# Kernel tuning notes

Hardware: AMD Instinct MI355X
Metric: run time of the kernel (lower is better)

## Reference

```python
import jax, jax.numpy as jnp
import numpy as np

B, T = 64, 256
IN, HID, OUT = 512, 1024, 256
NUM_DOMAINS = 20

def setup_inputs() -> dict:
    key = jax.random.key(0)
    k1, k2, k3, k4 = jax.random.split(key, 4)
    x = jax.random.normal(k1, (B, T, IN), dtype=jnp.float32)
    hetero_info = jax.random.randint(k2, (B, 2), 0, NUM_DOMAINS, dtype=jnp.int64)
    # embedding tables init N(0, 0.02) as in the torch module
    fc1_table = 0.02 * jax.random.normal(k3, (NUM_DOMAINS, IN * HID + HID), dtype=jnp.float32)
    fc2_table = 0.02 * jax.random.normal(k4, (NUM_DOMAINS, HID * OUT + OUT), dtype=jnp.float32)
    return {"x": x, "hetero_info": hetero_info, "fc1_table": fc1_table, "fc2_table": fc2_table}

def reference(x, hetero_info, fc1_table, fc2_table):
    domain_id = hetero_info[:, 0].astype(jnp.int32)
    Bn = domain_id.shape[0]
    fc1_param = fc1_table[domain_id]                     # (B, IN*HID + HID)
    w1 = fc1_param[:, : IN * HID].reshape(Bn, IN, HID)   # (B, IN, HID)
    b1 = fc1_param[:, IN * HID:].reshape(Bn, 1, HID)
    fc2_param = fc2_table[domain_id]                     # (B, HID*OUT + OUT)
    w2 = fc2_param[:, : HID * OUT].reshape(Bn, HID, OUT) # (B, HID, OUT)
    b2 = fc2_param[:, HID * OUT:].reshape(Bn, 1, OUT)
    h = jnp.einsum('bti,bih->bth', x, w1) + b1
    h = jax.nn.gelu(h, approximate=False)  # torch nn.GELU default = exact erf
    out = jnp.einsum('bth,bho->bto', h, w2) + b2
    return out
```

## Files before the change

### kernel.cpp

```cpp
#include <hip/hip_runtime.h>
#include <math.h>

#define B_  64
#define T_  256
#define IN_ 512
#define HID_ 1024
#define OUT_ 256
#define NDOM 20

typedef __bf16 bf16_t;
typedef __bf16 bf16x8 __attribute__((ext_vector_type(8)));
typedef float  f32x4  __attribute__((ext_vector_type(4)));

__device__ __forceinline__ unsigned f2bf_bits(float f) {
    unsigned u = __builtin_bit_cast(unsigned, f);
    return (u + 0x7FFFu + ((u >> 16) & 1u)) >> 16;
}
__device__ __forceinline__ unsigned pack_bf16x2(float x, float y) {
    return f2bf_bits(x) | (f2bf_bits(y) << 16);
}

__device__ __forceinline__ void gl_lds16(const void* g, void* l) {
    __builtin_amdgcn_global_load_lds(
        (const __attribute__((address_space(1))) unsigned*)g,
        (__attribute__((address_space(3))) unsigned*)l,
        16, 0, 0);
}

template<int K, int N>
__global__ __launch_bounds__(256) void cvt_transpose(
    const float* __restrict__ table, bf16_t* __restrict__ Wt, float* __restrict__ BiasOut)
{
    const int d  = blockIdx.z;
    const float* W = table + (size_t)d * ((size_t)K * N + N);
    const int n0 = blockIdx.x * 64;
    const int k0 = blockIdx.y * 64;
    const int tid = threadIdx.x;

    __shared__ float t[64][65];

    #pragma unroll
    for (int r = 0; r < 4; ++r) {
        const int kl = (tid >> 4) + r * 16;
        const int nl = (tid & 15) * 4;
        float4 v = *(const float4*)(W + (size_t)(k0 + kl) * N + n0 + nl);
        t[kl][nl + 0] = v.x; t[kl][nl + 1] = v.y;
        t[kl][nl + 2] = v.z; t[kl][nl + 3] = v.w;
    }
    __syncthreads();

    bf16_t* Wtd = Wt + (size_t)d * K * N;
    #pragma unroll
    for (int r = 0; r < 4; ++r) {
        const int nl = (tid >> 4) + r * 16;
        const int k4 = (tid & 15) * 4;
        uint2 p;
        p.x = pack_bf16x2(t[k4 + 0][nl], t[k4 + 1][nl]);
        p.y = pack_bf16x2(t[k4 + 2][nl], t[k4 + 3][nl]);
        *(uint2*)(Wtd + (size_t)(n0 + nl) * K + k0 + k4) = p;
    }

    if (blockIdx.y == 0 && tid < 64)
        BiasOut[(size_t)d * N + n0 + tid] = W[(size_t)K * N + n0 + tid];
}

__global__ __launch_bounds__(256) void fc1_gemm(
    const float*  __restrict__ X,
    const bf16_t* __restrict__ W1t,
    const float*  __restrict__ Bias,
    const int*    __restrict__ hetero,
    bf16_t*       __restrict__ H)
{
    const int id   = blockIdx.x;
    const int g    = id & 127;
    const int nidx = id >> 7;
    const int b    = g >> 1;
    const int m0   = (g & 1) * 128;
    const int n0   = nidx * 128;
    const int d    = hetero[2 * b];
    const bf16_t* W    = W1t + (size_t)d * HID_ * IN_;
    const float*  bias = Bias + (size_t)d * HID_;

    __shared__ __attribute__((aligned(16))) float  LdsA[128 * 32];
    __shared__ __attribute__((aligned(16))) bf16_t LdsB[128 * 32];

    const int tid  = threadIdx.x;
    const int wave = tid >> 6;
    const int lane = tid & 63;
    const int l16  = lane & 15;
    const int quad = lane >> 4;
    const int wm   = (wave >> 1) * 64;
    const int wn   = (wave & 1) * 64;

    f32x4 acc[4][4] = {};

    for (int kk = 0; kk < IN_; kk += 32) {
        #pragma unroll
        for (int cc = 0; cc < 4; ++cc) {
            const int r0  = wave * 32 + cc * 8;
            const int row = r0 + (lane >> 3);
            const int cs  = (lane & 7) ^ (row & 7);
            gl_lds16(X + ((size_t)(b * 256 + m0 + row) * IN_ + kk + cs * 4),
                     &LdsA[r0 * 32]);
        }
        #pragma unroll
        for (int cc = 0; cc < 2; ++cc) {
            const int r0  = wave * 32 + cc * 16;
            const int row = r0 + (lane >> 2);
            const int cs  = (lane & 3) ^ ((row >> 1) & 3);
            gl_lds16(W + (size_t)(n0 + row) * IN_ + kk + cs * 8,
                     &LdsB[r0 * 32]);
        }
        __syncthreads();

        bf16x8 af[4], bfg[4];
        #pragma unroll
        for (int i = 0; i < 4; ++i) {
            const int r  = wm + i * 16 + l16;
            const int c0 = (quad * 2)     ^ (r & 7);
            const int c1 = (quad * 2 + 1) ^ (r & 7);
            float4 f0 = *(const float4*)&LdsA[r * 32 + c0 * 4];
            float4 f1 = *(const float4*)&LdsA[r * 32 + c1 * 4];
            union { bf16x8 v; unsigned u[4]; } a;
            a.u[0] = pack_bf16x2(f0.x, f0.y);
            a.u[1] = pack_bf16x2(f0.z, f0.w);
            a.u[2] = pack_bf16x2(f1.x, f1.y);
            a.u[3] = pack_bf16x2(f1.z, f1.w);
            af[i] = a.v;
        }
        #pragma unroll
        for (int j = 0; j < 4; ++j) {
            const int r  = wn + j * 16 + l16;
            const int cB = quad ^ ((r >> 1) & 3);
            bfg[j] = *(const bf16x8*)&LdsB[r * 32 + cB * 8];
        }
        #pragma unroll
        for (int i = 0; i < 4; ++i)
            #pragma unroll
            for (int j = 0; j < 4; ++j)
                acc[i][j] = __builtin_amdgcn_mfma_f32_16x16x32_bf16(af[i], bfg[j], acc[i][j], 0, 0, 0);
        __syncthreads();
    }

    #pragma unroll
    for (int j = 0; j < 4; ++j) {
        const int n = n0 + wn + j * 16 + l16;
        const float bia = bias[n];
        #pragma unroll
        for (int i = 0; i < 4; ++i) {
            const int mbase = m0 + wm + i * 16 + quad * 4;
            #pragma unroll
            for (int r = 0; r < 4; ++r) {
                float vv = acc[i][j][r] + bia;
                vv = 0.5f * vv * (1.0f + erff(vv * 0.70710678f));
                H[((size_t)b * 256 + mbase + r) * HID_ + n] = (bf16_t)vv;
            }
        }
    }
}

__global__ __launch_bounds__(256) void fc2_gemm(
    const bf16_t* __restrict__ H,
    const bf16_t* __restrict__ W2t,
    const float*  __restrict__ Bias,
    const int*    __restrict__ hetero,
    float*        __restrict__ Out)
{
    const int id   = blockIdx.x;
    const int g    = id & 255;
    const int nidx = id >> 8;
    const int b    = g >> 2;
    const int m0   = (g & 3) * 64;
    const int n0   = nidx * 64;
    const int d    = hetero[2 * b];
    const bf16_t* W    = W2t + (size_t)d * OUT_ * HID_;
    const float*  bias = Bias + (size_t)d * OUT_;

    __shared__ __attribute__((aligned(16))) bf16_t LdsA[64 * 64];
    __shared__ __attribute__((aligned(16))) bf16_t LdsB[64 * 64];

    const int tid  = threadIdx.x;
    const int wave = tid >> 6;
    const int lane = tid & 63;
    const int l16  = lane & 15;
    const int quad = lane >> 4;
    const int wm   = (wave >> 1) * 32;
    const int wn   = (wave & 1) * 32;

    f32x4 acc[2][2] = {};

    for (int kk = 0; kk < HID_; kk += 64) {
        #pragma unroll
        for (int cc = 0; cc < 2; ++cc) {
            const int r0  = wave * 16 + cc * 8;
            const int row = r0 + (lane >> 3);
            const int cs  = (lane & 7) ^ (row & 7);
            gl_lds16(H + (size_t)(b * 256 + m0 + row) * HID_ + kk + cs * 8,
                     &LdsA[r0 * 64]);
        }
        #pragma unroll
        for (int cc = 0; cc < 2; ++cc) {
            const int r0  = wave * 16 + cc * 8;
            const int row = r0 + (lane >> 3);
            const int cs  = (lane & 7) ^ (row & 7);
            gl_lds16(W + (size_t)(n0 + row) * HID_ + kk + cs * 8,
                     &LdsB[r0 * 64]);
        }
        __syncthreads();

        #pragma unroll
        for (int h = 0; h < 2; ++h) {
            bf16x8 af[2], bfg[2];
            #pragma unroll
            for (int i = 0; i < 2; ++i) {
                const int r = wm + i * 16 + l16;
                const int c = (h * 4 + quad) ^ (r & 7);
                af[i] = *(const bf16x8*)&LdsA[r * 64 + c * 8];
            }
            #pragma unroll
            for (int j = 0; j < 2; ++j) {
                const int r = wn + j * 16 + l16;
                const int c = (h * 4 + quad) ^ (r & 7);
                bfg[j] = *(const bf16x8*)&LdsB[r * 64 + c * 8];
            }
            #pragma unroll
            for (int i = 0; i < 2; ++i)
                #pragma unroll
                for (int j = 0; j < 2; ++j)
                    acc[i][j] = __builtin_amdgcn_mfma_f32_16x16x32_bf16(af[i], bfg[j], acc[i][j], 0, 0, 0);
        }
        __syncthreads();
    }

    #pragma unroll
    for (int j = 0; j < 2; ++j) {
        const int n = n0 + wn + j * 16 + l16;
        const float bia = bias[n];
        #pragma unroll
        for (int i = 0; i < 2; ++i) {
            const int mbase = m0 + wm + i * 16 + quad * 4;
            #pragma unroll
            for (int r = 0; r < 4; ++r) {
                Out[((size_t)b * 256 + mbase + r) * OUT_ + n] = acc[i][j][r] + bia;
            }
        }
    }
}

extern "C" void kernel_launch(void* const* d_in, const int* in_sizes, int n_in,
                              void* d_out, int out_size, void* d_ws, size_t ws_size,
                              hipStream_t stream) {
    const float* x         = (const float*)d_in[0];
    const int*   hetero    = (const int*)d_in[1];
    const float* fc1_table = (const float*)d_in[2];
    const float* fc2_table = (const float*)d_in[3];
    float*       out       = (float*)d_out;

    char* ws = (char*)d_ws;
    bf16_t* W1t = (bf16_t*)(ws);
    bf16_t* W2t = (bf16_t*)(ws + 20971520);
    float*  b1  = (float*)(ws + 31457280);
    float*  b2  = (float*)(ws + 31539200);
    bf16_t* H   = (bf16_t*)(ws + 31559680);

    cvt_transpose<IN_, HID_><<<dim3(HID_ / 64, IN_ / 64, NDOM), 256, 0, stream>>>(
        fc1_table, W1t, b1);
    cvt_transpose<HID_, OUT_><<<dim3(OUT_ / 64, HID_ / 64, NDOM), 256, 0, stream>>>(
        fc2_table, W2t, b2);

    fc1_gemm<<<dim3(1024), 256, 0, stream>>>(x, W1t, b1, hetero, H);
    fc2_gemm<<<dim3(1024), 256, 0, stream>>>(H, W2t, b2, hetero, out);
}
```

Baseline: 193.1 us.

## Pre-convert X to bf16, deepen fc1 K tile, and vectorize GEMM epilogues

A new pass converts X to bf16 once, writing it into the output buffer as scratch. fc1 then loads bf16 A tiles with a K step of 64 instead of converting fp32 in its inner loop. Both GEMMs swap their MFMA operands so each lane holds four consecutive columns, which allows float4 bias loads and vector stores. fc1 also stages its GELU output through LDS so it can write coalesced 16-byte rows of H. The cost is an extra kernel launch plus a full read and write of X, and correctness depends on fc2 overwriting the output buffer after fc1 has consumed the scratch copy.

```diff
diff --git a/kernel.cpp b/kernel.cpp
--- a/kernel.cpp
+++ b/kernel.cpp
@@ -25,6 +25,17 @@
         (const __attribute__((address_space(1))) unsigned*)g,
         (__attribute__((address_space(3))) unsigned*)l,
         16, 0, 0);
+}
+
+__global__ __launch_bounds__(256) void cvt_x(
+    const float* __restrict__ X, bf16_t* __restrict__ Xbf)
+{
+    const size_t idx = (size_t)blockIdx.x * 256 + threadIdx.x;
+    float4 v = ((const float4*)X)[idx];
+    uint2 p;
+    p.x = pack_bf16x2(v.x, v.y);
+    p.y = pack_bf16x2(v.z, v.w);
+    ((uint2*)Xbf)[idx] = p;
 }
 
 template<int K, int N>
@@ -64,8 +75,9 @@
         BiasOut[(size_t)d * N + n0 + tid] = W[(size_t)K * N + n0 + tid];
 }
 
+#define CT_STRIDE 136
 __global__ __launch_bounds__(256) void fc1_gemm(
-    const float*  __restrict__ X,
+    const bf16_t* __restrict__ Xbf,
     const bf16_t* __restrict__ W1t,
     const float*  __restrict__ Bias,
     const int*    __restrict__ hetero,
@@ -80,9 +92,12 @@
     const int d    = hetero[2 * b];
     const bf16_t* W    = W1t + (size_t)d * HID_ * IN_;
     const float*  bias = Bias + (size_t)d * HID_;
-
-    __shared__ __attribute__((aligned(16))) float  LdsA[128 * 32];
-    __shared__ __attribute__((aligned(16))) bf16_t LdsB[128 * 32];
+    const bf16_t* A    = Xbf + (size_t)(b * 256 + m0) * IN_;
+
+    __shared__ __attribute__((aligned(16))) char smem[128 * CT_STRIDE * 2];
+    bf16_t* LdsA = (bf16_t*)smem;
+    bf16_t* LdsB = (bf16_t*)(smem + 16384);
+    bf16_t* Ct   = (bf16_t*)smem;
 
     const int tid  = threadIdx.x;
     const int wave = tid >> 6;
@@ -94,68 +109,76 @@
 
     f32x4 acc[4][4] = {};
 
-    for (int kk = 0; kk < IN_; kk += 32) {
+    for (int kk = 0; kk < IN_; kk += 64) {
         #pragma unroll
         for (int cc = 0; cc < 4; ++cc) {
             const int r0  = wave * 32 + cc * 8;
             const int row = r0 + (lane >> 3);
             const int cs  = (lane & 7) ^ (row & 7);
-            gl_lds16(X + ((size_t)(b * 256 + m0 + row) * IN_ + kk + cs * 4),
-                     &LdsA[r0 * 32]);
-        }
-        #pragma unroll
-        for (int cc = 0; cc < 2; ++cc) {
-            const int r0  = wave * 32 + cc * 16;
-            const int row = r0 + (lane >> 2);
-            const int cs  = (lane & 3) ^ ((row >> 1) & 3);
-            gl_lds16(W + (size_t)(n0 + row) * IN_ + kk + cs * 8,
-                     &LdsB[r0 * 32]);
+            gl_lds16(A + (size_t)row * IN_ + kk + cs * 8, &LdsA[r0 * 64]);
+        }
+        #pragma unroll
+        for (int cc = 0; cc < 4; ++cc) {
+            const int r0  = wave * 32 + cc * 8;
+            const int row = r0 + (lane >> 3);
+            const int cs  = (lane & 7) ^ (row & 7);
+            gl_lds16(W + (size_t)(n0 + row) * IN_ + kk + cs * 8, &LdsB[r0 * 64]);
         }
         __syncthreads();
 
-        bf16x8 af[4], bfg[4];
-        #pragma unroll
-        for (int i = 0; i < 4; ++i) {
-            const int r  = wm + i * 16 + l16;
-            const int c0 = (quad * 2)     ^ (r & 7);
-            const int c1 = (quad * 2 + 1) ^ (r & 7);
-            float4 f0 = *(const float4*)&LdsA[r * 32 + c0 * 4];
-            float4 f1 = *(const float4*)&LdsA[r * 32 + c1 * 4];
-            union { bf16x8 v; unsigned u[4]; } a;
-            a.u[0] = pack_bf16x2(f0.x, f0.y);
-            a.u[1] = pack_bf16x2(f0.z, f0.w);
-            a.u[2] = pack_bf16x2(f1.x, f1.y);
-            a.u[3] = pack_bf16x2(f1.z, f1.w);
-            af[i] = a.v;
-        }
+        #pragma unroll
+        for (int h = 0; h < 2; ++h) {
+            bf16x8 af[4], bfg[4];
+            #pragma unroll
+            for (int i = 0; i < 4; ++i) {
+                const int r = wm + i * 16 + l16;
+                const int c = (h * 4 + quad) ^ (r & 7);
+                af[i] = *(const bf16x8*)&LdsA[r * 64 + c * 8];
+            }
+            #pragma unroll
+            for (int j = 0; j < 4; ++j) {
+                const int r = wn + j * 16 + l16;
+                const int c = (h * 4 + quad) ^ (r & 7);
+                bfg[j] = *(const bf16x8*)&LdsB[r * 64 + c * 8];
+            }
+            #pragma unroll
+            for (int i = 0; i < 4; ++i)
+                #pragma unroll
+                for (int j = 0; j < 4; ++j)
+                    acc[i][j] = __builtin_amdgcn_mfma_f32_16x16x32_bf16(bfg[j], af[i], acc[i][j], 0, 0, 0);
+        }
+        __syncthreads();
+    }
+
+    #pragma unroll
+    for (int i = 0; i < 4; ++i) {
+        const int m = wm + i * 16 + l16;
         #pragma unroll
         for (int j = 0; j < 4; ++j) {
-            const int r  = wn + j * 16 + l16;
-            const int cB = quad ^ ((r >> 1) & 3);
-            bfg[j] = *(const bf16x8*)&LdsB[r * 32 + cB * 8];
-        }
-        #pragma unroll
-        for (int i = 0; i < 4; ++i)
-            #pragma unroll
-            for (int j = 0; j < 4; ++j)
-                acc[i][j] = __builtin_amdgcn_mfma_f32_16x16x32_bf16(af[i], bfg[j], acc[i][j], 0, 0, 0);
-        __syncthreads();
-    }
-
-    #pragma unroll
-    for (int j = 0; j < 4; ++j) {
-        const int n = n0 + wn + j * 16 + l16;
-        const float bia = bias[n];
-        #pragma unroll
-        for (int i = 0; i < 4; ++i) {
-            const int mbase = m0 + wm + i * 16 + quad * 4;
-            #pragma unroll
-            for (int r = 0; r < 4; ++r) {
-                float vv = acc[i][j][r] + bia;
-                vv = 0.5f * vv * (1.0f + erff(vv * 0.70710678f));
-                H[((size_t)b * 256 + mbase + r) * HID_ + n] = (bf16_t)vv;
-            }
-        }
+            const int nl = wn + j * 16 + quad * 4;
+            const float4 b4 = *(const float4*)&bias[n0 + nl];
+            float v0 = acc[i][j][0] + b4.x;
+            float v1 = acc[i][j][1] + b4.y;
+            float v2 = acc[i][j][2] + b4.z;
+            float v3 = acc[i][j][3] + b4.w;
+            v0 = 0.5f * v0 * (1.0f + erff(v0 * 0.70710678f));
+            v1 = 0.5f * v1 * (1.0f + erff(v1 * 0.70710678f));
+            v2 = 0.5f * v2 * (1.0f + erff(v2 * 0.70710678f));
+            v3 = 0.5f * v3 * (1.0f + erff(v3 * 0.70710678f));
+            uint2 p;
+            p.x = pack_bf16x2(v0, v1);
+            p.y = pack_bf16x2(v2, v3);
+            *(uint2*)&Ct[m * CT_STRIDE + nl] = p;
+        }
+    }
+    __syncthreads();
+
+    #pragma unroll
+    for (int it = 0; it < 8; ++it) {
+        const int row = it * 16 + (tid >> 4);
+        const int ch  = tid & 15;
+        uint4 v = *(const uint4*)&Ct[row * CT_STRIDE + ch * 8];
+        *(uint4*)&H[((size_t)(b * 256 + m0 + row)) * HID_ + n0 + ch * 8] = v;
     }
 }
 
@@ -227,22 +250,24 @@
             for (int i = 0; i < 2; ++i)
                 #pragma unroll
                 for (int j = 0; j < 2; ++j)
-                    acc[i][j] = __builtin_amdgcn_mfma_f32_16x16x32_bf16(af[i], bfg[j], acc[i][j], 0, 0, 0);
+                    acc[i][j] = __builtin_amdgcn_mfma_f32_16x16x32_bf16(bfg[j], af[i], acc[i][j], 0, 0, 0);
         }
         __syncthreads();
     }
 
     #pragma unroll
-    for (int j = 0; j < 2; ++j) {
-        const int n = n0 + wn + j * 16 + l16;
-        const float bia = bias[n];
-        #pragma unroll
-        for (int i = 0; i < 2; ++i) {
-            const int mbase = m0 + wm + i * 16 + quad * 4;
-            #pragma unroll
-            for (int r = 0; r < 4; ++r) {
-                Out[((size_t)b * 256 + mbase + r) * OUT_ + n] = acc[i][j][r] + bia;
-            }
+    for (int i = 0; i < 2; ++i) {
+        const int m = m0 + wm + i * 16 + l16;
+        #pragma unroll
+        for (int j = 0; j < 2; ++j) {
+            const int nl = wn + j * 16 + quad * 4;
+            const float4 b4 = *(const float4*)&bias[n0 + nl];
+            float4 o;
+            o.x = acc[i][j][0] + b4.x;
+            o.y = acc[i][j][1] + b4.y;
+            o.z = acc[i][j][2] + b4.z;
+            o.w = acc[i][j][3] + b4.w;
+            *(float4*)&Out[(size_t)(b * 256 + m) * OUT_ + n0 + nl] = o;
         }
     }
 }
@@ -263,11 +288,14 @@
     float*  b2  = (float*)(ws + 31539200);
     bf16_t* H   = (bf16_t*)(ws + 31559680);
 
+    bf16_t* Xbf = (bf16_t*)d_out;
+
+    cvt_x<<<dim3(8192), 256, 0, stream>>>(x, Xbf);
     cvt_transpose<IN_, HID_><<<dim3(HID_ / 64, IN_ / 64, NDOM), 256, 0, stream>>>(
         fc1_table, W1t, b1);
     cvt_transpose<HID_, OUT_><<<dim3(OUT_ / 64, HID_ / 64, NDOM), 256, 0, stream>>>(
         fc2_table, W2t, b2);
 
-    fc1_gemm<<<dim3(1024), 256, 0, stream>>>(x, W1t, b1, hetero, H);
+    fc1_gemm<<<dim3(1024), 256, 0, stream>>>(Xbf, W1t, b1, hetero, H);
     fc2_gemm<<<dim3(1024), 256, 0, stream>>>(H, W2t, b2, hetero, out);
 }
```

Result: faster. 188.6 us (-2.3%).
